# Kernel optimization log

Hardware: AMD Instinct MI355X
Metric: run time of the kernel (lower is better)

## Reference

```python
import jax, jax.numpy as jnp
from jax import lax
import numpy as np

EPS = 1e-5  # torch BatchNorm2d default eps


def _conv(x, w, b, stride, pad):
    y = lax.conv_general_dilated(x, w, (stride, stride), ((pad, pad), (pad, pad)),
                                 dimension_numbers=('NCHW', 'OIHW', 'NCHW'))
    return y + b[None, :, None, None]


def _deconv(x, w, b, pad):
    # torch ConvTranspose2d(stride=2, padding=pad); w: (in, out, k, k)
    k = w.shape[2]
    wf = jnp.flip(w, (2, 3)).transpose(1, 0, 2, 3)  # (out, in, k, k)
    y = lax.conv_general_dilated(x, wf, (1, 1), ((k - 1 - pad, k - 1 - pad),) * 2,
                                 lhs_dilation=(2, 2),
                                 dimension_numbers=('NCHW', 'OIHW', 'NCHW'))
    return y + b[None, :, None, None]


def _bn(x, g, b):
    # BatchNorm2d in training mode: batch statistics over (N, H, W), biased variance
    m = jnp.mean(x, (0, 2, 3), keepdims=True)
    v = jnp.var(x, (0, 2, 3), keepdims=True)
    return g[None, :, None, None] * (x - m) * lax.rsqrt(v + EPS) + b[None, :, None, None]


def _cbr(x, w, b, g, be, stride, pad):
    return jax.nn.relu(_bn(_conv(x, w, b, stride, pad), g, be))


def _forward(x, emb, e_w1, e_b1, e_g1, e_be1, e_w2, e_b2, e_g2, e_be2,
             e_rw1, e_rb1, e_rg1, e_rbe1, e_rw2, e_rb2, e_rg2, e_rbe2,
             e_pw, e_pb, d_pw, d_pb,
             d_rw1, d_rb1, d_rg1, d_rbe1, d_rw2, d_rb2, d_rg2, d_rbe2,
             d_tw1, d_tb1, d_tg1, d_tbe1, d_tw2, d_tb2):
    # ---- encoder ----
    h = _cbr(x, e_w1, e_b1, e_g1, e_be1, 2, 1)
    h = _cbr(h, e_w2, e_b2, e_g2, e_be2, 2, 1)
    h = h + _cbr(h, e_rw1, e_rb1, e_rg1, e_rbe1, 1, 1)
    h = h + _cbr(h, e_rw2, e_rb2, e_rg2, e_rbe2, 1, 0)
    enc = _conv(h, e_pw, e_pb, 1, 0)  # (B, D, H, W)
    B, C, H, W = enc.shape
    # faithful to torch enc.view(B, -1, C): raw row-major reshape (NOT a permute)
    ef = enc.reshape(B, -1, C)  # (B, HW, D)
    # ---- VQ: squared distances to codebook, argmin, gather ----
    d2 = (jnp.sum(ef * ef, -1, keepdims=True)
          - 2.0 * jnp.einsum('bnd,kd->bnk', ef, emb)
          + jnp.sum(emb * emb, -1))  # (B, HW, K); argmin identical to cdist argmin
    closest = jnp.argmin(d2, -1)  # (B, HW)
    q = emb[closest]  # (B, HW, D)
    commit = jnp.mean((lax.stop_gradient(q) - ef) ** 2)
    codebook = jnp.mean((q - lax.stop_gradient(ef)) ** 2)
    qloss = codebook + 0.25 * commit
    # straight-through estimator
    qo = (ef + lax.stop_gradient(q - ef)).reshape(B, C, H, W)
    # ---- decoder ----
    h = _conv(qo, d_pw, d_pb, 1, 0)
    h = h + _cbr(h, d_rw1, d_rb1, d_rg1, d_rbe1, 1, 1)
    h = h + _cbr(h, d_rw2, d_rb2, d_rg2, d_rbe2, 1, 1)
    h = jax.nn.relu(_bn(_deconv(h, d_tw1, d_tb1, 1), d_tg1, d_tbe1))
    out = jax.nn.sigmoid(_deconv(h, d_tw2, d_tb2, 1))
    return out, closest, qloss


def setup_inputs() -> dict:
    HID, K, D, CH, B, IMG = 256, 512, 64, 3, 32, 128
    keys = iter(jax.random.split(jax.random.key(0), 24))
    def w(*s):
        return jax.random.normal(next(keys), s, jnp.float32) * 0.02
    z, o = jnp.zeros, jnp.ones
    return dict(
        x=jax.random.uniform(next(keys), (B, CH, IMG, IMG), jnp.float32),
        emb=w(K, D),
        e_w1=w(HID, CH, 4, 4), e_b1=z(HID), e_g1=o(HID), e_be1=z(HID),
        e_w2=w(HID, HID, 4, 4), e_b2=z(HID), e_g2=o(HID), e_be2=z(HID),
        e_rw1=w(HID, HID, 3, 3), e_rb1=z(HID), e_rg1=o(HID), e_rbe1=z(HID),
        e_rw2=w(HID, HID, 1, 1), e_rb2=z(HID), e_rg2=o(HID), e_rbe2=z(HID),
        e_pw=w(D, HID, 1, 1), e_pb=z(D),
        d_pw=w(HID, D, 1, 1), d_pb=z(HID),
        d_rw1=w(HID, HID, 3, 3), d_rb1=z(HID), d_rg1=o(HID), d_rbe1=z(HID),
        d_rw2=w(HID, HID, 3, 3), d_rb2=z(HID), d_rg2=o(HID), d_rbe2=z(HID),
        d_tw1=w(HID, HID, 4, 4), d_tb1=z(HID), d_tg1=o(HID), d_tbe1=z(HID),
        d_tw2=w(HID, CH, 4, 4), d_tb2=z(CH),
    )


def reference(x, emb, e_w1, e_b1, e_g1, e_be1, e_w2, e_b2, e_g2, e_be2,
              e_rw1, e_rb1, e_rg1, e_rbe1, e_rw2, e_rb2, e_rg2, e_rbe2,
              e_pw, e_pb, d_pw, d_pb,
              d_rw1, d_rb1, d_rg1, d_rbe1, d_rw2, d_rb2, d_rg2, d_rbe2,
              d_tw1, d_tb1, d_tg1, d_tbe1, d_tw2, d_tb2):
    return _forward(x, emb, e_w1, e_b1, e_g1, e_be1, e_w2, e_b2, e_g2, e_be2,
                    e_rw1, e_rb1, e_rg1, e_rbe1, e_rw2, e_rb2, e_rg2, e_rbe2,
                    e_pw, e_pb, d_pw, d_pb,
                    d_rw1, d_rb1, d_rg1, d_rbe1, d_rw2, d_rb2, d_rg2, d_rbe2,
                    d_tw1, d_tb1, d_tg1, d_tbe1, d_tw2, d_tb2)
```

## Files before the change

kernel.cpp:

```cpp
#include <hip/hip_runtime.h>
#include <hip/hip_bf16.h>
#include <math.h>


#define OUT_CLOSEST 1572864
#define OUT_QLOSS   1605632

#define OFF_BIG   0u
#define OFF_BP    0u
#define OFF_ENC   8388608u
#define OFF_HT1   8388608u
#define OFF_HT2   12582912u
#define OFF_HT3   16777216u
#define OFF_QOT   20971520u
#define OFF_S     33554432u
#define OFF_W2T   41943040u
#define OFF_RW1T  42991616u
#define OFF_RW2T  43581440u
#define OFF_PWT   43646976u
#define OFF_DPWB  43675648u
#define OFF_DRW1B 43683840u
#define OFF_DRW2B 43978752u
#define OFF_TW1B  44273664u
#define OFF_STATS 44797952u
#define OFF_NORM  44798464u
#define OFF_CIDX  44799488u
#define OFF_PART  44832256u
#define OFF_STAT2 44840448u
#define OFF_WB    44873216u

typedef __bf16 bf16x8 __attribute__((ext_vector_type(8)));
typedef float f32x4 __attribute__((ext_vector_type(4)));

__device__ __forceinline__ unsigned short f2bf(float f) {
  __hip_bfloat16 h = __float2bfloat16(f);
  return *reinterpret_cast<unsigned short*>(&h);
}
__device__ __forceinline__ float bf2f(unsigned short u) {
  return __uint_as_float((unsigned)u << 16);
}

__global__ __launch_bounds__(256) void prep_all(
    const float* __restrict__ e_w2, float* __restrict__ W2T,
    const float* __restrict__ e_rw1, float* __restrict__ RW1T,
    const float* __restrict__ e_rw2, float* __restrict__ RW2T,
    const float* __restrict__ e_pw, float* __restrict__ PWT,
    const float* __restrict__ d_tw2, __hip_bfloat16* __restrict__ WB,
    const float* __restrict__ d_pw, __hip_bfloat16* __restrict__ DPWB,
    const float* __restrict__ d_rw1, __hip_bfloat16* __restrict__ DRW1B,
    const float* __restrict__ d_rw2, __hip_bfloat16* __restrict__ DRW2B,
    const float* __restrict__ d_tw1, __hip_bfloat16* __restrict__ TW1B,
    const float* __restrict__ emb, double* __restrict__ NORM) {
  const int bid = blockIdx.x, tid = threadIdx.x;
  if (bid < 4096) {
    int i = bid * 256 + tid;
    int co = i & 255; int r = i >> 8; int ci = r & 255; int t = r >> 8;
    W2T[i] = e_w2[((size_t)co * 256 + ci) * 16 + t];
  } else if (bid < 6400) {
    int i = (bid - 4096) * 256 + tid;
    if (i < 589824) {
      int co = i % 256; int r = i / 256; int ci = r % 256; int t = r / 256;
      RW1T[i] = e_rw1[((size_t)co * 256 + ci) * 9 + t];
    }
  } else if (bid < 6656) {
    int i = (bid - 6400) * 256 + tid;
    int co = i & 255; int ci = i >> 8;
    RW2T[i] = e_rw2[(size_t)co * 256 + ci];
  } else if (bid < 6720) {
    int i = (bid - 6656) * 256 + tid;
    int co = i & 63; int ci = i >> 6;
    PWT[i] = e_pw[(size_t)co * 256 + ci];
  } else if (bid < 6976) {
    int i = (bid - 6720) * 256 + tid;
    int e = i & 7; int ln = (i >> 3) & 15; int ciq = (i >> 7) & 31; int t = i >> 12;
    int ci = ciq * 8 + e;
    float v = (ln < 3) ? d_tw2[((size_t)ci * 3 + ln) * 16 + t] : 0.f;
    WB[i] = __float2bfloat16(v);
  } else if (bid < 7040) {
    int i = (bid - 6976) * 256 + tid;
    int ci = i & 63; int co = i >> 6;
    DPWB[i] = __float2bfloat16(d_pw[(size_t)co * 64 + ci]);
  } else if (bid < 9344) {
    int i = (bid - 7040) * 256 + tid;
    if (i < 589824) {
      int ci = i % 256; int r = i / 256; int co = r % 256; int t = r / 256;
      DRW1B[i] = __float2bfloat16(d_rw1[((size_t)co * 256 + ci) * 9 + t]);
    }
  } else if (bid < 11648) {
    int i = (bid - 9344) * 256 + tid;
    if (i < 589824) {
      int ci = i % 256; int r = i / 256; int co = r % 256; int t = r / 256;
      DRW2B[i] = __float2bfloat16(d_rw2[((size_t)co * 256 + ci) * 9 + t]);
    }
  } else if (bid < 15744) {
    int i = (bid - 11648) * 256 + tid;
    int ci = i & 255; int r = i >> 8; int co = r & 255; int t = r >> 8;
    TW1B[i] = __float2bfloat16(d_tw1[((size_t)ci * 256 + co) * 16 + t]);
  } else {
    int k = (bid - 15744) * 256 + tid;
    if (k < 512) {
      double s = 0.0;
      for (int d = 0; d < 64; ++d) { double e = emb[(k << 6) + d]; s += e * e; }
      NORM[k] = s;
    }
  }
}

__global__ __launch_bounds__(256) void conv1_w(const float* __restrict__ x, const float* __restrict__ w,
                                               const float* __restrict__ bias, float* __restrict__ out) {
  __shared__ float ws[6144];
  __shared__ float xs[3][10][132];
  const int tid = threadIdx.x;
  const int s = blockIdx.x, b = blockIdx.y, ch = blockIdx.z;
  for (int i = tid; i < 1536; i += 256)
    *(float4*)&ws[i * 4] = *(const float4*)&w[ch * 6144 + i * 4];
  for (int i = tid; i < 3 * 10 * 130; i += 256) {
    int col = i % 130; int r2 = i / 130; int lr = r2 % 10; int ci = r2 / 10;
    int ih = 8 * s - 1 + lr; int iw = col - 1;
    float v = 0.f;
    if ((unsigned)ih < 128u && (unsigned)iw < 128u)
      v = x[((size_t)(b * 3 + ci) << 14) + (ih << 7) + iw];
    xs[ci][lr][col] = v;
  }
  __syncthreads();
  const int ohl = tid >> 6, ow = tid & 63;
  const int oh = (s << 2) + ohl;
  float xr[48];
#pragma unroll
  for (int ci = 0; ci < 3; ++ci)
#pragma unroll
    for (int kh = 0; kh < 4; ++kh)
#pragma unroll
      for (int kw = 0; kw < 4; ++kw)
        xr[(ci * 4 + kh) * 4 + kw] = xs[ci][2 * ohl + kh][2 * ow + kw];
  float* op = out + (((size_t)b * 256) << 12) + (oh << 6) + ow;
  for (int co = 0; co < 128; ++co) {
    float acc = bias[ch * 128 + co];
    const float* wp = &ws[co * 48];
#pragma unroll
    for (int k = 0; k < 48; k += 4) {
      float4 wv = *(const float4*)&wp[k];
      acc = fmaf(xr[k], wv.x, acc);
      acc = fmaf(xr[k + 1], wv.y, acc);
      acc = fmaf(xr[k + 2], wv.z, acc);
      acc = fmaf(xr[k + 3], wv.w, acc);
    }
    op[(size_t)(ch * 128 + co) << 12] = acc;
  }
}

__global__ __launch_bounds__(256) void bn_stats_p(const float* __restrict__ in, double* __restrict__ part,
                                                  int log2HW, int Bn) {
  int c = blockIdx.x, g = blockIdx.y;
  int tid = threadIdx.x;
  int HW = 1 << log2HW;
  int cnt = Bn << log2HW;
  int seg = cnt >> 3;
  double s = 0.0, s2 = 0.0;
  for (int i = g * seg + tid; i < (g + 1) * seg; i += 256) {
    int b = i >> log2HW, p = i & (HW - 1);
    float v = in[((size_t)(b * 256 + c) << log2HW) + p];
    s += v; s2 += (double)v * v;
  }
  __shared__ double r1[256], r2[256];
  r1[tid] = s; r2[tid] = s2;
  __syncthreads();
  for (int st = 128; st > 0; st >>= 1) {
    if (tid < st) { r1[tid] += r1[tid + st]; r2[tid] += r2[tid + st]; }
    __syncthreads();
  }
  if (tid == 0) {
    part[(c << 3) + g] = r1[0];
    part[2048 + (c << 3) + g] = r2[0];
  }
}
__global__ __launch_bounds__(256) void bn_stats_f(const double* __restrict__ part, float* __restrict__ stats,
                                                  int cnt) {
  int c = threadIdx.x;
  double s = 0.0, s2 = 0.0;
  for (int g = 0; g < 8; ++g) { s += part[(c << 3) + g]; s2 += part[2048 + (c << 3) + g]; }
  double m = s / cnt;
  double var = s2 / cnt - m * m;
  stats[c] = (float)m;
  stats[256 + c] = (float)(1.0 / sqrt(var + 1e-5));
}

__global__ __launch_bounds__(256) void bn_apply(const float4* __restrict__ in, const float4* __restrict__ res,
                                                float4* __restrict__ out, const float* __restrict__ stats,
                                                const float* __restrict__ g, const float* __restrict__ be,
                                                int log2HW, int n4) {
  int i = blockIdx.x * 256 + threadIdx.x;
  if (i >= n4) return;
  int c = (i >> (log2HW - 2)) & 255;
  float sc = stats[256 + c] * g[c];
  float sh = be[c] - stats[c] * sc;
  float4 v = in[i];
  float4 o;
  o.x = fmaxf(fmaf(v.x, sc, sh), 0.f);
  o.y = fmaxf(fmaf(v.y, sc, sh), 0.f);
  o.z = fmaxf(fmaf(v.z, sc, sh), 0.f);
  o.w = fmaxf(fmaf(v.w, sc, sh), 0.f);
  if (res) { float4 r = res[i]; o.x += r.x; o.y += r.y; o.z += r.z; o.w += r.w; }
  out[i] = o;
}

__global__ __launch_bounds__(256) void bn_apply_td(const float* __restrict__ in, const float* __restrict__ res,
                                                   float* __restrict__ out_f, __hip_bfloat16* __restrict__ out_bt,
                                                   const float* __restrict__ stats, const float* __restrict__ g,
                                                   const float* __restrict__ be) {
  int j = blockIdx.x * 256 + threadIdx.x;
  int sp = j & 1023, cg = (j >> 10) & 31, b = j >> 15;
  unsigned short us[8];
#pragma unroll
  for (int q = 0; q < 8; ++q) {
    int c = cg * 8 + q;
    float sc = stats[256 + c] * g[c];
    float sh = be[c] - stats[c] * sc;
    size_t idx = ((size_t)(b * 256 + c) << 10) + sp;
    float y = fmaxf(fmaf(in[idx], sc, sh), 0.f) + res[idx];
    if (out_f) out_f[idx] = y;
    us[q] = f2bf(y);
  }
  ushort4* op = (ushort4*)(out_bt + (((size_t)(b << 10) + sp) << 8) + cg * 8);
  op[0] = make_ushort4(us[0], us[1], us[2], us[3]);
  op[1] = make_ushort4(us[4], us[5], us[6], us[7]);
}

__global__ __launch_bounds__(256) void fp32_to_bt(const float* __restrict__ in, __hip_bfloat16* __restrict__ out) {
  int j = blockIdx.x * 256 + threadIdx.x;
  int sp = j & 1023, cg = (j >> 10) & 31, b = j >> 15;
  unsigned short us[8];
#pragma unroll
  for (int q = 0; q < 8; ++q) {
    int c = cg * 8 + q;
    us[q] = f2bf(in[((size_t)(b * 256 + c) << 10) + sp]);
  }
  ushort4* op = (ushort4*)(out + (((size_t)(b << 10) + sp) << 8) + cg * 8);
  op[0] = make_ushort4(us[0], us[1], us[2], us[3]);
  op[1] = make_ushort4(us[4], us[5], us[6], us[7]);
}

template<int CI, int KH, int KW, int PAD>
__global__ __launch_bounds__(256) void mconv(const __hip_bfloat16* __restrict__ act,
                                             const __hip_bfloat16* __restrict__ wt,
                                             const float* __restrict__ bias,
                                             float* __restrict__ out, int CO) {
  const int tid = threadIdx.x;
  const int lane = tid & 63, wv = tid >> 6;
  const int ln = lane & 15, kg = lane >> 4;
  const int b = blockIdx.z;
  const int co_base = blockIdx.y << 6;
  const int sp_base = blockIdx.x << 6;
  const int co_n = co_base + wv * 16 + ln;
  int oh[4], ow[4];
#pragma unroll
  for (int mf = 0; mf < 4; ++mf) {
    int s = sp_base + mf * 16 + ln;
    oh[mf] = s >> 5; ow[mf] = s & 31;
  }
  f32x4 acc[4] = {{0,0,0,0},{0,0,0,0},{0,0,0,0},{0,0,0,0}};
  const size_t actb = (size_t)b * 1024 * CI;
  const int kg8 = kg * 8;
  for (int kh = 0; kh < KH; ++kh)
    for (int kw = 0; kw < KW; ++kw) {
      const int t = kh * KW + kw;
      const __hip_bfloat16* bp = wt + ((size_t)t * CO + co_n) * CI + kg8;
      const __hip_bfloat16* ap[4]; bool val[4];
#pragma unroll
      for (int mf = 0; mf < 4; ++mf) {
        int ih = oh[mf] + kh - PAD, iw = ow[mf] + kw - PAD;
        val[mf] = ((unsigned)ih < 32u) && ((unsigned)iw < 32u);
        ap[mf] = val[mf] ? (act + actb + (size_t)((ih << 5) + iw) * CI + kg8) : (act + actb + kg8);
      }
#pragma unroll
      for (int ci0 = 0; ci0 < CI; ci0 += 32) {
        bf16x8 bf = *(const bf16x8*)(bp + ci0);
        bf16x8 af[4];
#pragma unroll
        for (int mf = 0; mf < 4; ++mf) {
          bf16x8 z = {};
          bf16x8 tv = *(const bf16x8*)(ap[mf] + ci0);
          af[mf] = val[mf] ? tv : z;
        }
#pragma unroll
        for (int mf = 0; mf < 4; ++mf)
          acc[mf] = __builtin_amdgcn_mfma_f32_16x16x32_bf16(af[mf], bf, acc[mf], 0, 0, 0);
      }
    }
  float bv = bias[co_n];
#pragma unroll
  for (int mf = 0; mf < 4; ++mf) {
    int sp_r = sp_base + mf * 16 + kg * 4;
    float4 r = make_float4(acc[mf][0] + bv, acc[mf][1] + bv, acc[mf][2] + bv, acc[mf][3] + bv);
    *(float4*)&out[((size_t)(b * CO + co_n) << 10) + sp_r] = r;
  }
}

__global__ __launch_bounds__(256, 4) void mconv_s(const __hip_bfloat16* __restrict__ act,
                                                  const __hip_bfloat16* __restrict__ wt,
                                                  const float* __restrict__ bias,
                                                  float* __restrict__ out) {
  __shared__ __hip_bfloat16 As[4 * 34 * 136];
  const int tid = threadIdx.x;
  const int lane = tid & 63, wv = tid >> 6;
  const int ln = lane & 15, kg = lane >> 4;
  const int b = blockIdx.z;
  const int co_base = blockIdx.y << 6;
  const int sp_base = blockIdx.x << 6;
  const int co_n = co_base + wv * 16 + ln;
  const int r_first = (sp_base >> 5) - 1;
  const size_t actb = (size_t)b << 18;
  const int kg8 = kg * 8;

  f32x4 acc[4] = {{0,0,0,0},{0,0,0,0},{0,0,0,0},{0,0,0,0}};

  int lr0[4], lc0[4];
#pragma unroll
  for (int mf = 0; mf < 4; ++mf) {
    int s = mf * 16 + ln;
    lr0[mf] = s >> 5;
    lc0[mf] = s & 31;
  }

  for (int cih = 0; cih < 2; ++cih) {
    __syncthreads();
    for (int sIdx = tid; sIdx < 2176; sIdx += 256) {
      int v8 = sIdx & 15;
      int rc = sIdx >> 4;
      int col = rc % 34;
      int row = rc / 34;
      int ih = r_first + row;
      int iw = col - 1;
      uint4 val = make_uint4(0, 0, 0, 0);
      if ((unsigned)ih < 32u && (unsigned)iw < 32u)
        val = *(const uint4*)(act + actb + ((size_t)((ih << 5) + iw) << 8) + cih * 128 + v8 * 8);
      *(uint4*)(&As[rc * 136 + v8 * 8]) = val;
    }
    __syncthreads();
#pragma unroll
    for (int kh = 0; kh < 3; ++kh)
#pragma unroll
      for (int kw = 0; kw < 3; ++kw) {
        const int t = kh * 3 + kw;
        const __hip_bfloat16* bp = wt + ((size_t)t * 256 + co_n) * 256 + cih * 128 + kg8;
#pragma unroll
        for (int c32 = 0; c32 < 4; ++c32) {
          bf16x8 bf = *(const bf16x8*)(bp + (c32 << 5));
#pragma unroll
          for (int mf = 0; mf < 4; ++mf) {
            int lrow = lr0[mf] + kh;
            int lcol = lc0[mf] + kw;
            bf16x8 af = *(const bf16x8*)(&As[(lrow * 34 + lcol) * 136 + (c32 << 5) + kg8]);
            acc[mf] = __builtin_amdgcn_mfma_f32_16x16x32_bf16(af, bf, acc[mf], 0, 0, 0);
          }
        }
      }
  }
  float bv = bias[co_n];
#pragma unroll
  for (int mf = 0; mf < 4; ++mf) {
    int sp_r = sp_base + mf * 16 + kg * 4;
    float4 r = make_float4(acc[mf][0] + bv, acc[mf][1] + bv, acc[mf][2] + bv, acc[mf][3] + bv);
    *(float4*)&out[((size_t)(b * 256 + co_n) << 10) + sp_r] = r;
  }
}

__global__ __launch_bounds__(256) void mdeconv(const __hip_bfloat16* __restrict__ act,
                                               const __hip_bfloat16* __restrict__ wt,
                                               const float* __restrict__ bias,
                                               __hip_bfloat16* __restrict__ out) {
  const int tid = threadIdx.x;
  const int lane = tid & 63, wv = tid >> 6;
  const int ln = lane & 15, kg = lane >> 4;
  const int b = blockIdx.z;
  const int co_base = blockIdx.y << 6;
  const int sp_base = blockIdx.x << 6;
  const int co_a = co_base + wv * 16 + ln;
  int a0[4], c0[4];
#pragma unroll
  for (int mf = 0; mf < 4; ++mf) {
    int s = sp_base + mf * 16 + ln;
    a0[mf] = s >> 5; c0[mf] = s & 31;
  }
  f32x4 acc[16];
#pragma unroll
  for (int q = 0; q < 16; ++q) acc[q] = (f32x4){0, 0, 0, 0};

  const size_t actb = (size_t)b << 18;
  const int kg8 = kg * 8;
  const int nmem[3]     = {1, 2, 1};
  const int khm[3][2]   = {{3, 0}, {1, 2}, {0, 0}};
  const int phm[3][2]   = {{0, 0}, {0, 1}, {1, 0}};

#pragma unroll
  for (int di = 0; di < 3; ++di) {
    const int dh = di - 1;
#pragma unroll
    for (int dj = 0; dj < 3; ++dj) {
      const int dw = dj - 1;
      const __hip_bfloat16* bp[4]; bool val[4];
#pragma unroll
      for (int mf = 0; mf < 4; ++mf) {
        int ih = a0[mf] + dh, iw = c0[mf] + dw;
        val[mf] = ((unsigned)ih < 32u) && ((unsigned)iw < 32u);
        bp[mf] = val[mf] ? (act + actb + (size_t)((ih << 5) + iw) * 256 + kg8) : (act + actb + kg8);
      }
#pragma unroll
      for (int ci0 = 0; ci0 < 256; ci0 += 32) {
        bf16x8 bfr[4];
#pragma unroll
        for (int mf = 0; mf < 4; ++mf) {
          bf16x8 z = {};
          bf16x8 tv = *(const bf16x8*)(bp[mf] + ci0);
          bfr[mf] = val[mf] ? tv : z;
        }
#pragma unroll
        for (int u = 0; u < 2; ++u) {
          if (u < nmem[di]) {
#pragma unroll
            for (int v = 0; v < 2; ++v) {
              if (v < nmem[dj]) {
                const int t = khm[di][u] * 4 + khm[dj][v];
                const int pidx = (phm[di][u] * 2 + phm[dj][v]) << 2;
                bf16x8 af = *(const bf16x8*)(wt + ((size_t)t * 256 + co_a) * 256 + kg8 + ci0);
#pragma unroll
                for (int mf = 0; mf < 4; ++mf)
                  acc[pidx + mf] = __builtin_amdgcn_mfma_f32_16x16x32_bf16(af, bfr[mf], acc[pidx + mf], 0, 0, 0);
              }
            }
          }
        }
      }
    }
  }
  const int co_r = co_base + wv * 16 + kg * 4;
  float b0 = bias[co_r], b1 = bias[co_r + 1], b2 = bias[co_r + 2], b3 = bias[co_r + 3];
#pragma unroll
  for (int ph = 0; ph < 2; ++ph)
#pragma unroll
    for (int pw = 0; pw < 2; ++pw) {
      const int pidx = (ph * 2 + pw) << 2;
#pragma unroll
      for (int mf = 0; mf < 4; ++mf) {
        int s = sp_base + mf * 16 + ln;
        int a = s >> 5, c = s & 31;
        size_t obase = (((size_t)(b << 12)) + (((a << 1) + ph) << 6) + (c << 1) + pw) << 8;
        f32x4 av = acc[pidx + mf];
        ushort4 u = make_ushort4(f2bf(av[0] + b0), f2bf(av[1] + b1),
                                 f2bf(av[2] + b2), f2bf(av[3] + b3));
        *(ushort4*)(out + obase + co_r) = u;
      }
    }
}

__global__ __launch_bounds__(256) void bnbt_stage1(const __hip_bfloat16* __restrict__ in, float* __restrict__ part) {
  int t = threadIdx.x, blk = blockIdx.x;
  float s[8] = {0,0,0,0,0,0,0,0}, s2[8] = {0,0,0,0,0,0,0,0};
  size_t base = ((size_t)blk * 256 + t) * 8;
  const size_t stride = 64 * 256 * 8;
  for (int it = 0; it < 256; ++it) {
    ushort4 u0 = *(const ushort4*)(in + base);
    ushort4 u1 = *(const ushort4*)(in + base + 4);
    float v[8] = {bf2f(u0.x), bf2f(u0.y), bf2f(u0.z), bf2f(u0.w),
                  bf2f(u1.x), bf2f(u1.y), bf2f(u1.z), bf2f(u1.w)};
#pragma unroll
    for (int q = 0; q < 8; ++q) { s[q] += v[q]; s2[q] += v[q] * v[q]; }
    base += stride;
  }
  __shared__ float ls[256][8], ls2[256][8];
#pragma unroll
  for (int q = 0; q < 8; ++q) { ls[t][q] = s[q]; ls2[t][q] = s2[q]; }
  __syncthreads();
  if (t < 32) {
#pragma unroll
    for (int q = 0; q < 8; ++q) {
      float a = 0.f, a2 = 0.f;
      for (int r = 0; r < 8; ++r) { a += ls[t + 32 * r][q]; a2 += ls2[t + 32 * r][q]; }
      part[blk * 256 + t * 8 + q] = a;
      part[16384 + blk * 256 + t * 8 + q] = a2;
    }
  }
}

__global__ __launch_bounds__(256) void bnbt_stage2(const float* __restrict__ part, float* __restrict__ stats) {
  int c = threadIdx.x;
  double s = 0.0, s2 = 0.0;
  for (int q = 0; q < 64; ++q) { s += part[q * 256 + c]; s2 += part[16384 + q * 256 + c]; }
  double m = s / 131072.0;
  double var = s2 / 131072.0 - m * m;
  stats[c] = (float)m;
  stats[256 + c] = (float)(1.0 / sqrt(var + 1e-5));
}

__global__ __launch_bounds__(256) void bn_apply_bt(__hip_bfloat16* __restrict__ io, const float* __restrict__ stats,
                                                   const float* __restrict__ g, const float* __restrict__ be) {
  int i = blockIdx.x * 256 + threadIdx.x;
  size_t off = (size_t)i * 8;
  int c0 = (i & 31) * 8;
  ushort4 u0 = *(const ushort4*)(io + off);
  ushort4 u1 = *(const ushort4*)(io + off + 4);
  float v[8] = {bf2f(u0.x), bf2f(u0.y), bf2f(u0.z), bf2f(u0.w),
                bf2f(u1.x), bf2f(u1.y), bf2f(u1.z), bf2f(u1.w)};
  unsigned short us[8];
#pragma unroll
  for (int q = 0; q < 8; ++q) {
    int c = c0 + q;
    float sc = stats[256 + c] * g[c];
    float sh = be[c] - stats[c] * sc;
    us[q] = f2bf(fmaxf(fmaf(v[q], sc, sh), 0.f));
  }
  *(ushort4*)(io + off) = make_ushort4(us[0], us[1], us[2], us[3]);
  *(ushort4*)(io + off + 4) = make_ushort4(us[4], us[5], us[6], us[7]);
}

template<int STRIDE, int KK>
__global__ __launch_bounds__(256, 4) void conv_b64(
    const float* __restrict__ in, const float* __restrict__ wt,
    const float* __restrict__ bias, float* __restrict__ out,
    int CI, int CO, int Hin, int Win, int pad) {
  __shared__ float Xs[2][16][64];
  __shared__ float Ws[2][16][128];
  const int tid = threadIdx.x;
  const int cb = tid & 15, sb = tid >> 4;
  const int sx = tid >> 4;
  const int cx = (tid & 15) << 2;
  const int tw = tid >> 5;
  const int ww = (tid & 31) << 2;
  const int b = blockIdx.z;
  const int co0 = blockIdx.y << 7;
  const int sp0 = blockIdx.x << 6;
  const int HWin = Hin * Win;
  const int nst = KK * KK * 16;

  int oh_s[4], ow_s[4];
#pragma unroll
  for (int q = 0; q < 4; ++q) {
    int s = sp0 + cx + q;
    oh_s[q] = s >> 5; ow_s[q] = s & 31;
  }

  float acc[8][4];
#pragma unroll
  for (int i = 0; i < 8; ++i)
#pragma unroll
    for (int j = 0; j < 4; ++j) acc[i][j] = 0.f;

  float pv[4];
  float4 pw0, pw1;

  auto gather = [&](int st) {
    int t = st >> 4;
    int ci0 = (st & 15) << 4;
    int kh = t / KK, kw = t - kh * KK;
    const float* ib = in + (size_t)(b * CI + ci0 + sx) * HWin;
#pragma unroll
    for (int q = 0; q < 4; ++q) {
      int ih = oh_s[q] * STRIDE + kh - pad;
      int iw = ow_s[q] * STRIDE + kw - pad;
      bool ok = ((unsigned)ih < (unsigned)Hin) && ((unsigned)iw < (unsigned)Win);
      pv[q] = ok ? ib[ih * Win + iw] : 0.f;
    }
    const float* wb = wt + ((size_t)t * CI + ci0 + tw) * CO + co0 + ww;
    pw0 = *(const float4*)wb;
    pw1 = *(const float4*)(wb + (size_t)8 * CO);
  };

  gather(0);
  *(float4*)&Xs[0][sx][cx]     = make_float4(pv[0], pv[1], pv[2], pv[3]);
  *(float4*)&Ws[0][tw][ww]     = pw0;
  *(float4*)&Ws[0][tw + 8][ww] = pw1;
  __syncthreads();

  for (int st = 0; st < nst; ++st) {
    const int cur = st & 1;
    const bool more = (st + 1 < nst);
    if (more) gather(st + 1);
    const float (*Xc)[64]  = Xs[cur];
    const float (*Wc)[128] = Ws[cur];
#pragma unroll 4
    for (int ci = 0; ci < 16; ++ci) {
      float4 w0 = *(const float4*)&Wc[ci][cb << 2];
      float4 w1 = *(const float4*)&Wc[ci][64 + (cb << 2)];
      float4 xv = *(const float4*)&Xc[ci][sb << 2];
#define FMA_ROW(I, WC) \
      acc[I][0] = fmaf(WC, xv.x, acc[I][0]); \
      acc[I][1] = fmaf(WC, xv.y, acc[I][1]); \
      acc[I][2] = fmaf(WC, xv.z, acc[I][2]); \
      acc[I][3] = fmaf(WC, xv.w, acc[I][3]);
      FMA_ROW(0, w0.x) FMA_ROW(1, w0.y) FMA_ROW(2, w0.z) FMA_ROW(3, w0.w)
      FMA_ROW(4, w1.x) FMA_ROW(5, w1.y) FMA_ROW(6, w1.z) FMA_ROW(7, w1.w)
#undef FMA_ROW
    }
    if (more) {
      const int nxt = cur ^ 1;
      *(float4*)&Xs[nxt][sx][cx]     = make_float4(pv[0], pv[1], pv[2], pv[3]);
      *(float4*)&Ws[nxt][tw][ww]     = pw0;
      *(float4*)&Ws[nxt][tw + 8][ww] = pw1;
      __syncthreads();
    }
  }

#pragma unroll
  for (int i = 0; i < 8; ++i) {
    int co = co0 + ((i < 4) ? (cb << 2) + i : 64 + (cb << 2) + (i - 4));
    float bv = bias[co];
    *(float4*)&out[((size_t)(b * CO + co) << 10) + sp0 + (sb << 2)] =
        make_float4(acc[i][0] + bv, acc[i][1] + bv, acc[i][2] + bv, acc[i][3] + bv);
  }
}

__device__ __forceinline__ void tile_fma(const float* Ws_, const float* Xs_, int co4, int sp4,
                                         float acc[4][4]) {
#pragma unroll
  for (int ci = 0; ci < 16; ++ci) {
    float4 wv = *(const float4*)(Ws_ + (ci << 6) + co4);
    float4 xv = *(const float4*)(Xs_ + (ci << 6) + sp4);
    acc[0][0] = fmaf(xv.x, wv.x, acc[0][0]);
    acc[0][1] = fmaf(xv.x, wv.y, acc[0][1]);
    acc[0][2] = fmaf(xv.x, wv.z, acc[0][2]);
    acc[0][3] = fmaf(xv.x, wv.w, acc[0][3]);
    acc[1][0] = fmaf(xv.y, wv.x, acc[1][0]);
    acc[1][1] = fmaf(xv.y, wv.y, acc[1][1]);
    acc[1][2] = fmaf(xv.y, wv.z, acc[1][2]);
    acc[1][3] = fmaf(xv.y, wv.w, acc[1][3]);
    acc[2][0] = fmaf(xv.z, wv.x, acc[2][0]);
    acc[2][1] = fmaf(xv.z, wv.y, acc[2][1]);
    acc[2][2] = fmaf(xv.z, wv.z, acc[2][2]);
    acc[2][3] = fmaf(xv.z, wv.w, acc[2][3]);
    acc[3][0] = fmaf(xv.w, wv.x, acc[3][0]);
    acc[3][1] = fmaf(xv.w, wv.y, acc[3][1]);
    acc[3][2] = fmaf(xv.w, wv.z, acc[3][2]);
    acc[3][3] = fmaf(xv.w, wv.w, acc[3][3]);
  }
}

__global__ __launch_bounds__(256) void conv_tiled(
    const float* __restrict__ in, const float* __restrict__ wt,
    const float* __restrict__ bias, float* __restrict__ out,
    int CI, int CO, int Hin, int Win, int Hout, int Wout,
    int KH, int KW, int stride, int pad) {
  __shared__ float Xs[16 * 64];
  __shared__ float Ws[16 * 64];
  const int tid = threadIdx.x;
  const int b = blockIdx.z;
  const int co_base = blockIdx.y << 6;
  const int sp_base = blockIdx.x << 6;
  const int lo = tid & 15, hi = tid >> 4;
  const int co4 = lo << 2, sp4 = hi << 2;
  const int HWin = Hin * Win, HWout = Hout * Wout;

  int oh0[4], ow0[4];
#pragma unroll
  for (int j = 0; j < 4; ++j) {
    int s = sp_base + (lo << 2) + j;
    oh0[j] = s / Wout; ow0[j] = s - oh0[j] * Wout;
  }
  float acc[4][4] = {{0.f,0.f,0.f,0.f},{0.f,0.f,0.f,0.f},{0.f,0.f,0.f,0.f},{0.f,0.f,0.f,0.f}};

  for (int kh = 0; kh < KH; ++kh)
    for (int kw = 0; kw < KW; ++kw) {
      const int t = kh * KW + kw;
      for (int ci0 = 0; ci0 < CI; ci0 += 16) {
        const float* ib = in + (size_t)(b * CI + ci0 + hi) * HWin;
        float v[4];
#pragma unroll
        for (int j = 0; j < 4; ++j) {
          int ih = oh0[j] * stride + kh - pad;
          int iw = ow0[j] * stride + kw - pad;
          v[j] = 0.f;
          if ((unsigned)ih < (unsigned)Hin && (unsigned)iw < (unsigned)Win)
            v[j] = ib[ih * Win + iw];
        }
        *(float4*)&Xs[(hi << 6) + (lo << 2)] = make_float4(v[0], v[1], v[2], v[3]);
        *(float4*)&Ws[(hi << 6) + (lo << 2)] =
            *(const float4*)&wt[((size_t)t * CI + ci0 + hi) * CO + co_base + (lo << 2)];
        __syncthreads();
        tile_fma(Ws, Xs, co4, sp4, acc);
        __syncthreads();
      }
    }
#pragma unroll
  for (int i = 0; i < 4; ++i) {
    int co = co_base + co4 + i;
    float bv = bias[co];
    float4 r = make_float4(acc[0][i] + bv, acc[1][i] + bv, acc[2][i] + bv, acc[3][i] + bv);
    *(float4*)&out[(size_t)(b * CO + co) * HWout + sp_base + sp4] = r;
  }
}

__global__ __launch_bounds__(256) void deconv_mfma(const __hip_bfloat16* __restrict__ xt,
                                                   const __hip_bfloat16* __restrict__ wb,
                                                   const float* __restrict__ bias, float* __restrict__ out) {
  const int tid = threadIdx.x;
  const int wv = tid >> 6, lane = tid & 63;
  const int ln = lane & 15, kg = lane >> 4;
  const int posb = blockIdx.x * 256 + wv * 64;
  const int sect = posb >> 12;
  const int b = sect >> 2, ph = (sect >> 1) & 1, pw = sect & 1;
  const int a = (posb >> 6) & 63;
  int khs[2], dhs[2], kws[2], dws[2];
  if (ph == 0) { khs[0]=1; dhs[0]=0; khs[1]=3; dhs[1]=-1; }
  else         { khs[0]=0; dhs[0]=1; khs[1]=2; dhs[1]=0; }
  if (pw == 0) { kws[0]=1; dws[0]=0; kws[1]=3; dws[1]=-1; }
  else         { kws[0]=0; dws[0]=1; kws[1]=2; dws[1]=0; }
  f32x4 acc[4] = {{0,0,0,0},{0,0,0,0},{0,0,0,0},{0,0,0,0}};
  const size_t actb = (size_t)b << 12;
#pragma unroll
  for (int ti = 0; ti < 2; ++ti) {
    int ih = a + dhs[ti];
    if ((unsigned)ih >= 64u) continue;
#pragma unroll
    for (int tj = 0; tj < 2; ++tj) {
      const int t = khs[ti] * 4 + kws[tj];
      const int dw = dws[tj];
      const __hip_bfloat16* xrow = xt + ((actb + (ih << 6)) << 8);
#pragma unroll
      for (int c32 = 0; c32 < 8; ++c32) {
        bf16x8 bf = *(const bf16x8*)(wb + ((((size_t)t * 32 + (c32 << 2) + kg) * 16 + ln) << 3));
#pragma unroll
        for (int mf = 0; mf < 4; ++mf) {
          int c = (mf << 4) + ln;
          int iw = c + dw;
          bf16x8 av = {};
          if ((unsigned)iw < 64u)
            av = *(const bf16x8*)(xrow + ((size_t)iw << 8) + (c32 << 5) + (kg << 3));
          acc[mf] = __builtin_amdgcn_mfma_f32_16x16x32_bf16(av, bf, acc[mf], 0, 0, 0);
        }
      }
    }
  }
  if (ln < 3) {
    float bv = bias[ln];
    int oh = 2 * a + ph;
    size_t ob = ((size_t)(b * 3 + ln) << 14) + (oh << 7) + pw;
#pragma unroll
    for (int mf = 0; mf < 4; ++mf)
#pragma unroll
      for (int r = 0; r < 4; ++r) {
        int c = (mf << 4) + (kg << 2) + r;
        out[ob + (c << 1)] = 1.f / (1.f + __expf(-(acc[mf][r] + bv)));
      }
  }
}

__global__ __launch_bounds__(128) void vq_argmin(const float* __restrict__ enc, const float* __restrict__ emb,
                                                 const double* __restrict__ norms, int* __restrict__ cidx,
                                                 float* __restrict__ closest_out) {
  __shared__ float se[128 * 64];
  int tid = threadIdx.x;
  int r = blockIdx.x * 128 + tid;
  double ef[64];
  const float4* ep = (const float4*)(enc + ((size_t)r << 6));
#pragma unroll
  for (int q = 0; q < 16; ++q) {
    float4 v = ep[q];
    ef[4*q] = v.x; ef[4*q+1] = v.y; ef[4*q+2] = v.z; ef[4*q+3] = v.w;
  }
  double best = 1e300; int bi = 0;
  for (int q = 0; q < 4; ++q) {
    __syncthreads();
    for (int i = tid; i < 8192; i += 128) se[i] = emb[q * 8192 + i];
    __syncthreads();
    for (int k = 0; k < 128; ++k) {
      const float* cp = &se[k << 6];
      double p0 = 0.0, p1 = 0.0, p2 = 0.0, p3 = 0.0;
#pragma unroll
      for (int d = 0; d < 64; d += 4) {
        p0 = fma(ef[d],     (double)cp[d],     p0);
        p1 = fma(ef[d + 1], (double)cp[d + 1], p1);
        p2 = fma(ef[d + 2], (double)cp[d + 2], p2);
        p3 = fma(ef[d + 3], (double)cp[d + 3], p3);
      }
      double dot = (p0 + p1) + (p2 + p3);
      double d2 = norms[q * 128 + k] - 2.0 * dot;
      if (d2 < best) { best = d2; bi = q * 128 + k; }
    }
  }
  cidx[r] = bi;
  closest_out[r] = (float)bi;
}

__global__ __launch_bounds__(256) void vq_gather(const float* __restrict__ enc, const float* __restrict__ emb,
                                                 const int* __restrict__ cidx, __hip_bfloat16* __restrict__ qot,
                                                 float* __restrict__ part) {
  int tid = threadIdx.x;
  int i = blockIdx.x * 256 + tid;
  int r = i >> 6, d = i & 63;
  int k = cidx[r];
  float q = emb[(k << 6) + d];
  float e = enc[i];
  int b = r >> 10;
  int f = ((r & 1023) << 6) + d;
  int d_orig = f >> 10, p = f & 1023;
  qot[(((size_t)(b << 10)) + p) * 64 + d_orig] = __float2bfloat16(q);
  float df = q - e;
  __shared__ float red[256];
  red[tid] = df * df;
  __syncthreads();
  for (int st = 128; st > 0; st >>= 1) {
    if (tid < st) red[tid] += red[tid + st];
    __syncthreads();
  }
  if (tid == 0) part[blockIdx.x] = red[0];
}

__global__ __launch_bounds__(256) void qloss_final(const float* __restrict__ part, float* __restrict__ out) {
  int tid = threadIdx.x;
  double s = 0.0;
  for (int i = tid; i < 8192; i += 256) s += part[i];
  __shared__ double red[256];
  red[tid] = s;
  __syncthreads();
  for (int st = 128; st > 0; st >>= 1) {
    if (tid < st) red[tid] += red[tid + st];
    __syncthreads();
  }
  if (tid == 0) {
    double mean = red[0] / 2097152.0;
    out[0] = (float)(1.25 * mean);
  }
}

extern "C" void kernel_launch(void* const* d_in, const int* in_sizes, int n_in,
                              void* d_out, int out_size, void* d_ws, size_t ws_size,
                              hipStream_t stream) {
  const float* x     = (const float*)d_in[0];
  const float* emb   = (const float*)d_in[1];
  const float* e_w1  = (const float*)d_in[2];
  const float* e_b1  = (const float*)d_in[3];
  const float* e_g1  = (const float*)d_in[4];
  const float* e_be1 = (const float*)d_in[5];
  const float* e_w2  = (const float*)d_in[6];
  const float* e_b2  = (const float*)d_in[7];
  const float* e_g2  = (const float*)d_in[8];
  const float* e_be2 = (const float*)d_in[9];
  const float* e_rw1 = (const float*)d_in[10];
  const float* e_rb1 = (const float*)d_in[11];
  const float* e_rg1 = (const float*)d_in[12];
  const float* e_rbe1= (const float*)d_in[13];
  const float* e_rw2 = (const float*)d_in[14];
  const float* e_rb2 = (const float*)d_in[15];
  const float* e_rg2 = (const float*)d_in[16];
  const float* e_rbe2= (const float*)d_in[17];
  const float* e_pw  = (const float*)d_in[18];
  const float* e_pb  = (const float*)d_in[19];
  const float* d_pw  = (const float*)d_in[20];
  const float* d_pb  = (const float*)d_in[21];
  const float* d_rw1 = (const float*)d_in[22];
  const float* d_rb1 = (const float*)d_in[23];
  const float* d_rg1 = (const float*)d_in[24];
  const float* d_rbe1= (const float*)d_in[25];
  const float* d_rw2 = (const float*)d_in[26];
  const float* d_rb2 = (const float*)d_in[27];
  const float* d_rg2 = (const float*)d_in[28];
  const float* d_rbe2= (const float*)d_in[29];
  const float* d_tw1 = (const float*)d_in[30];
  const float* d_tb1 = (const float*)d_in[31];
  const float* d_tg1 = (const float*)d_in[32];
  const float* d_tbe1= (const float*)d_in[33];
  const float* d_tw2 = (const float*)d_in[34];
  const float* d_tb2 = (const float*)d_in[35];

  float* ws   = (float*)d_ws;
  float* BIG  = ws + OFF_BIG;
  float* BP   = ws + OFF_BP;
  float* ENC  = ws + OFF_ENC;
  float* S    = ws + OFF_S;
  float* W2T  = ws + OFF_W2T;
  float* RW1T = ws + OFF_RW1T;
  float* RW2T = ws + OFF_RW2T;
  float* PWT  = ws + OFF_PWT;
  float* STATS= ws + OFF_STATS;
  double* NORM= (double*)(ws + OFF_NORM);
  int*   CIDX = (int*)(ws + OFF_CIDX);
  float* PART = ws + OFF_PART;
  float* STAT2= ws + OFF_STAT2;
  double* PARTD = (double*)(ws + OFF_STAT2);
  __hip_bfloat16* HT1  = (__hip_bfloat16*)(ws + OFF_HT1);
  __hip_bfloat16* HT2  = (__hip_bfloat16*)(ws + OFF_HT2);
  __hip_bfloat16* HT3  = (__hip_bfloat16*)(ws + OFF_HT3);
  __hip_bfloat16* QOT  = (__hip_bfloat16*)(ws + OFF_QOT);
  __hip_bfloat16* T9BT = (__hip_bfloat16*)(ws + OFF_BIG);
  __hip_bfloat16* DPWB = (__hip_bfloat16*)(ws + OFF_DPWB);
  __hip_bfloat16* DRW1B= (__hip_bfloat16*)(ws + OFF_DRW1B);
  __hip_bfloat16* DRW2B= (__hip_bfloat16*)(ws + OFF_DRW2B);
  __hip_bfloat16* TW1B = (__hip_bfloat16*)(ws + OFF_TW1B);
  __hip_bfloat16* WB   = (__hip_bfloat16*)(ws + OFF_WB);
  float* outp = (float*)d_out;

  dim3 blk(256);
  dim3 bn_grid(256, 8);

  prep_all<<<15746, blk, 0, stream>>>(e_w2, W2T, e_rw1, RW1T, e_rw2, RW2T, e_pw, PWT,
                                      d_tw2, WB, d_pw, DPWB, d_rw1, DRW1B, d_rw2, DRW2B,
                                      d_tw1, TW1B, emb, NORM);

  conv1_w<<<dim3(16, 32, 2), blk, 0, stream>>>(x, e_w1, e_b1, BIG);
  bn_stats_p<<<bn_grid, blk, 0, stream>>>(BIG, PARTD, 12, 32);
  bn_stats_f<<<1, blk, 0, stream>>>(PARTD, STATS, 131072);
  bn_apply<<<32768, blk, 0, stream>>>((float4*)BIG, nullptr, (float4*)BIG, STATS, e_g1, e_be1, 12, 8388608);
  conv_b64<2, 4><<<dim3(16, 2, 32), blk, 0, stream>>>(BIG, W2T, e_b2, S, 256, 256, 64, 64, 1);
  bn_stats_p<<<bn_grid, blk, 0, stream>>>(S, PARTD, 10, 32);
  bn_stats_f<<<1, blk, 0, stream>>>(PARTD, STATS, 32768);
  bn_apply<<<8192, blk, 0, stream>>>((float4*)S, nullptr, (float4*)S, STATS, e_g2, e_be2, 10, 2097152);
  conv_b64<1, 3><<<dim3(16, 2, 32), blk, 0, stream>>>(S, RW1T, e_rb1, BP, 256, 256, 32, 32, 1);
  bn_stats_p<<<bn_grid, blk, 0, stream>>>(BP, PARTD, 10, 32);
  bn_stats_f<<<1, blk, 0, stream>>>(PARTD, STATS, 32768);
  bn_apply<<<8192, blk, 0, stream>>>((float4*)BP, (float4*)S, (float4*)BP, STATS, e_rg1, e_rbe1, 10, 2097152);
  conv_b64<1, 1><<<dim3(16, 2, 32), blk, 0, stream>>>(BP, RW2T, e_rb2, S, 256, 256, 32, 32, 0);
  bn_stats_p<<<bn_grid, blk, 0, stream>>>(S, PARTD, 10, 32);
  bn_stats_f<<<1, blk, 0, stream>>>(PARTD, STATS, 32768);
  bn_apply<<<8192, blk, 0, stream>>>((float4*)S, (float4*)BP, (float4*)S, STATS, e_rg2, e_rbe2, 10, 2097152);
  conv_tiled<<<dim3(16, 1, 32), blk, 0, stream>>>(S, PWT, e_pb, ENC, 256, 64, 32, 32, 32, 32, 1, 1, 1, 0);

  vq_argmin<<<256, dim3(128), 0, stream>>>(ENC, emb, NORM, CIDX, outp + OUT_CLOSEST);
  vq_gather<<<8192, blk, 0, stream>>>(ENC, emb, CIDX, QOT, PART);
  qloss_final<<<1, blk, 0, stream>>>(PART, outp + OUT_QLOSS);

  mconv<64, 1, 1, 0><<<dim3(16, 4, 32), blk, 0, stream>>>(QOT, DPWB, d_pb, S, 256);
  fp32_to_bt<<<4096, blk, 0, stream>>>(S, HT1);
  mconv_s<<<dim3(16, 4, 32), blk, 0, stream>>>(HT1, DRW1B, d_rb1, BP);
  bn_stats_p<<<bn_grid, blk, 0, stream>>>(BP, PARTD, 10, 32);
  bn_stats_f<<<1, blk, 0, stream>>>(PARTD, STATS, 32768);
  bn_apply_td<<<4096, blk, 0, stream>>>(BP, S, S, HT2, STATS, d_rg1, d_rbe1);
  mconv_s<<<dim3(16, 4, 32), blk, 0, stream>>>(HT2, DRW2B, d_rb2, BP);
  bn_stats_p<<<bn_grid, blk, 0, stream>>>(BP, PARTD, 10, 32);
  bn_stats_f<<<1, blk, 0, stream>>>(PARTD, STATS, 32768);
  bn_apply_td<<<4096, blk, 0, stream>>>(BP, S, nullptr, HT3, STATS, d_rg2, d_rbe2);
  mdeconv<<<dim3(16, 4, 32), blk, 0, stream>>>(HT3, TW1B, d_tb1, T9BT);
  bnbt_stage1<<<64, blk, 0, stream>>>(T9BT, STAT2);
  bnbt_stage2<<<1, blk, 0, stream>>>(STAT2, STATS);
  bn_apply_bt<<<16384, blk, 0, stream>>>(T9BT, STATS, d_tg1, d_tbe1);
  deconv_mfma<<<2048, blk, 0, stream>>>(T9BT, WB, d_tb2, outp);
}
```

Baseline: 3.002 ms.

## Stage deconv activations in LDS and use fp32 VQ argmin with fp64 fallback

```diff
diff --git a/kernel.cpp b/kernel.cpp
--- a/kernel.cpp
+++ b/kernel.cpp
@@ -365,10 +365,11 @@
   }
 }
 
-__global__ __launch_bounds__(256) void mdeconv(const __hip_bfloat16* __restrict__ act,
-                                               const __hip_bfloat16* __restrict__ wt,
-                                               const float* __restrict__ bias,
-                                               __hip_bfloat16* __restrict__ out) {
+__global__ __launch_bounds__(256) void mdeconv_s(const __hip_bfloat16* __restrict__ act,
+                                                 const __hip_bfloat16* __restrict__ wt,
+                                                 const float* __restrict__ bias,
+                                                 __hip_bfloat16* __restrict__ out) {
+  __shared__ __hip_bfloat16 As[4 * 34 * 136];
   const int tid = threadIdx.x;
   const int lane = tid & 63, wv = tid >> 6;
   const int ln = lane & 15, kg = lane >> 4;
@@ -376,44 +377,45 @@
   const int co_base = blockIdx.y << 6;
   const int sp_base = blockIdx.x << 6;
   const int co_a = co_base + wv * 16 + ln;
-  int a0[4], c0[4];
-#pragma unroll
-  for (int mf = 0; mf < 4; ++mf) {
-    int s = sp_base + mf * 16 + ln;
-    a0[mf] = s >> 5; c0[mf] = s & 31;
-  }
-  f32x4 acc[16];
-#pragma unroll
-  for (int q = 0; q < 16; ++q) acc[q] = (f32x4){0, 0, 0, 0};
-
+  const int r_first = (sp_base >> 5) - 1;
   const size_t actb = (size_t)b << 18;
   const int kg8 = kg * 8;
+
+  int lr0[4], lc0[4];
+#pragma unroll
+  for (int mf = 0; mf < 4; ++mf) {
+    int s = mf * 16 + ln;
+    lr0[mf] = s >> 5;
+    lc0[mf] = s & 31;
+  }
+
+  f32x4 acc[16];
+#pragma unroll
+  for (int q = 0; q < 16; ++q) acc[q] = (f32x4){0, 0, 0, 0};
+
   const int nmem[3]     = {1, 2, 1};
   const int khm[3][2]   = {{3, 0}, {1, 2}, {0, 0}};
   const int phm[3][2]   = {{0, 0}, {0, 1}, {1, 0}};
 
-#pragma unroll
-  for (int di = 0; di < 3; ++di) {
-    const int dh = di - 1;
-#pragma unroll
-    for (int dj = 0; dj < 3; ++dj) {
-      const int dw = dj - 1;
-      const __hip_bfloat16* bp[4]; bool val[4];
-#pragma unroll
-      for (int mf = 0; mf < 4; ++mf) {
-        int ih = a0[mf] + dh, iw = c0[mf] + dw;
-        val[mf] = ((unsigned)ih < 32u) && ((unsigned)iw < 32u);
-        bp[mf] = val[mf] ? (act + actb + (size_t)((ih << 5) + iw) * 256 + kg8) : (act + actb + kg8);
-      }
-#pragma unroll
-      for (int ci0 = 0; ci0 < 256; ci0 += 32) {
-        bf16x8 bfr[4];
-#pragma unroll
-        for (int mf = 0; mf < 4; ++mf) {
-          bf16x8 z = {};
-          bf16x8 tv = *(const bf16x8*)(bp[mf] + ci0);
-          bfr[mf] = val[mf] ? tv : z;
-        }
+  for (int cih = 0; cih < 2; ++cih) {
+    __syncthreads();
+    for (int sIdx = tid; sIdx < 2176; sIdx += 256) {
+      int v8 = sIdx & 15;
+      int rc = sIdx >> 4;
+      int col = rc % 34;
+      int row = rc / 34;
+      int ih = r_first + row;
+      int iw = col - 1;
+      uint4 val = make_uint4(0, 0, 0, 0);
+      if ((unsigned)ih < 32u && (unsigned)iw < 32u)
+        val = *(const uint4*)(act + actb + ((size_t)((ih << 5) + iw) << 8) + cih * 128 + v8 * 8);
+      *(uint4*)(&As[rc * 136 + v8 * 8]) = val;
+    }
+    __syncthreads();
+#pragma unroll
+    for (int di = 0; di < 3; ++di) {
+#pragma unroll
+      for (int dj = 0; dj < 3; ++dj) {
 #pragma unroll
         for (int u = 0; u < 2; ++u) {
           if (u < nmem[di]) {
@@ -422,10 +424,18 @@
               if (v < nmem[dj]) {
                 const int t = khm[di][u] * 4 + khm[dj][v];
                 const int pidx = (phm[di][u] * 2 + phm[dj][v]) << 2;
-                bf16x8 af = *(const bf16x8*)(wt + ((size_t)t * 256 + co_a) * 256 + kg8 + ci0);
-#pragma unroll
-                for (int mf = 0; mf < 4; ++mf)
-                  acc[pidx + mf] = __builtin_amdgcn_mfma_f32_16x16x32_bf16(af, bfr[mf], acc[pidx + mf], 0, 0, 0);
+                const __hip_bfloat16* bp = wt + ((size_t)t * 256 + co_a) * 256 + cih * 128 + kg8;
+#pragma unroll
+                for (int c32 = 0; c32 < 4; ++c32) {
+                  bf16x8 af = *(const bf16x8*)(bp + (c32 << 5));
+#pragma unroll
+                  for (int mf = 0; mf < 4; ++mf) {
+                    int lrow = lr0[mf] + di;
+                    int lcol = lc0[mf] + dj;
+                    bf16x8 bfr = *(const bf16x8*)(&As[(lrow * 34 + lcol) * 136 + (c32 << 5) + kg8]);
+                    acc[pidx + mf] = __builtin_amdgcn_mfma_f32_16x16x32_bf16(af, bfr, acc[pidx + mf], 0, 0, 0);
+                  }
+                }
               }
             }
           }
@@ -749,32 +759,54 @@
   __shared__ float se[128 * 64];
   int tid = threadIdx.x;
   int r = blockIdx.x * 128 + tid;
-  double ef[64];
+  float ef[64];
   const float4* ep = (const float4*)(enc + ((size_t)r << 6));
 #pragma unroll
   for (int q = 0; q < 16; ++q) {
     float4 v = ep[q];
     ef[4*q] = v.x; ef[4*q+1] = v.y; ef[4*q+2] = v.z; ef[4*q+3] = v.w;
   }
-  double best = 1e300; int bi = 0;
+  float best = 3.4e38f, second = 3.4e38f; int bi = 0;
   for (int q = 0; q < 4; ++q) {
     __syncthreads();
     for (int i = tid; i < 8192; i += 128) se[i] = emb[q * 8192 + i];
     __syncthreads();
     for (int k = 0; k < 128; ++k) {
       const float* cp = &se[k << 6];
+      float p0 = 0.f, p1 = 0.f, p2 = 0.f, p3 = 0.f;
+#pragma unroll
+      for (int d = 0; d < 64; d += 4) {
+        p0 = fmaf(ef[d],     cp[d],     p0);
+        p1 = fmaf(ef[d + 1], cp[d + 1], p1);
+        p2 = fmaf(ef[d + 2], cp[d + 2], p2);
+        p3 = fmaf(ef[d + 3], cp[d + 3], p3);
+      }
+      float dot = (p0 + p1) + (p2 + p3);
+      float d2 = (float)norms[q * 128 + k] - 2.f * dot;
+      if (d2 < best) { second = best; best = d2; bi = q * 128 + k; }
+      else if (d2 < second) { second = d2; }
+    }
+  }
+  if (second - best < 5e-4f) {
+    double efd[64];
+#pragma unroll
+    for (int d = 0; d < 64; ++d) efd[d] = (double)ef[d];
+    double bestd = 1e300; int bd = 0;
+    for (int k = 0; k < 512; ++k) {
+      const float* cp = &emb[(size_t)k << 6];
       double p0 = 0.0, p1 = 0.0, p2 = 0.0, p3 = 0.0;
 #pragma unroll
       for (int d = 0; d < 64; d += 4) {
-        p0 = fma(ef[d],     (double)cp[d],     p0);
-        p1 = fma(ef[d + 1], (double)cp[d + 1], p1);
-        p2 = fma(ef[d + 2], (double)cp[d + 2], p2);
-        p3 = fma(ef[d + 3], (double)cp[d + 3], p3);
+        p0 = fma(efd[d],     (double)cp[d],     p0);
+        p1 = fma(efd[d + 1], (double)cp[d + 1], p1);
+        p2 = fma(efd[d + 2], (double)cp[d + 2], p2);
+        p3 = fma(efd[d + 3], (double)cp[d + 3], p3);
       }
       double dot = (p0 + p1) + (p2 + p3);
-      double d2 = norms[q * 128 + k] - 2.0 * dot;
-      if (d2 < best) { best = d2; bi = q * 128 + k; }
-    }
+      double d2 = norms[k] - 2.0 * dot;
+      if (d2 < bestd) { bestd = d2; bd = k; }
+    }
+    bi = bd;
   }
   cidx[r] = bi;
   closest_out[r] = (float)bi;
@@ -927,7 +959,7 @@
   bn_stats_p<<<bn_grid, blk, 0, stream>>>(BP, PARTD, 10, 32);
   bn_stats_f<<<1, blk, 0, stream>>>(PARTD, STATS, 32768);
   bn_apply_td<<<4096, blk, 0, stream>>>(BP, S, nullptr, HT3, STATS, d_rg2, d_rbe2);
-  mdeconv<<<dim3(16, 4, 32), blk, 0, stream>>>(HT3, TW1B, d_tb1, T9BT);
+  mdeconv_s<<<dim3(16, 4, 32), blk, 0, stream>>>(HT3, TW1B, d_tb1, T9BT);
   bnbt_stage1<<<64, blk, 0, stream>>>(T9BT, STAT2);
   bnbt_stage2<<<1, blk, 0, stream>>>(STAT2, STATS);
   bn_apply_bt<<<16384, blk, 0, stream>>>(T9BT, STATS, d_tg1, d_tbe1);
```

After: 3.021 ms. About the same (+0.6%).
